# Optimization experiments

Hardware: AMD Instinct MI355X
Metric: run time of the kernel (lower is better)

The kernel has to match this reference:

```python
import jax, jax.numpy as jnp
import numpy as np

B, N, LQ, DK, DV, DD = 2, 16, 512, 64, 64, 128
TEMPERATURE = 8.0  # sqrt(DK)
NEG_INF = -1e9


def setup_inputs() -> dict:
    key = jax.random.key(0)
    ks = jax.random.split(key, 9)
    h2 = 2 * DD  # dc hidden width = d0 + d1
    return {
        "q": jax.random.normal(ks[0], (B, N, LQ, DK), jnp.float32),
        "k": jax.random.normal(ks[1], (B, N, LQ, DK), jnp.float32),
        "v": jax.random.normal(ks[2], (B, N, LQ, DV), jnp.float32),
        "d0": jax.random.normal(ks[3], (B, LQ, DD), jnp.float32),
        "d1": jax.random.normal(ks[4], (B, LQ, DD), jnp.float32),
        "W1": jax.random.normal(ks[5], (h2, h2), jnp.float32) / np.sqrt(h2),
        "b1": jnp.zeros((h2,), jnp.float32),
        "W2": jax.random.normal(ks[6], (h2, 2), jnp.float32) / np.sqrt(h2),
        "b2": jnp.zeros((2,), jnp.float32),
    }


def reference(q, k, v, d0, d1, W1, b1, W2, b2):
    b, n, lq, dk = q.shape
    dd = d0.shape[-1]
    # pairwise features: f[b,i,j] = concat(d0[b,i], d1[b,j])  -> [b,lq,lq,2dd]
    f = jnp.concatenate(
        [
            jnp.broadcast_to(d0[:, :, None, :], (b, lq, lq, dd)),
            jnp.broadcast_to(d1[:, None, :, :], (b, lq, lq, dd)),
        ],
        axis=-1,
    )
    h = jax.nn.relu(jnp.einsum("bijf,fg->bijg", f, W1) + b1)
    logits = jnp.einsum("bijg,gc->bijc", h, W2) + b2  # [b,lq,lq,2]
    # eval-mode gumbel_softmax(hard=True, tau=1, training=False): argmax of logits
    decisions = (jnp.argmax(logits, axis=-1) == 1)[:, None, :, :]  # [b,1,lq,lq]
    attn = jnp.einsum("bnid,bnjd->bnij", q / TEMPERATURE, k)
    attn = jnp.where(decisions, attn, NEG_INF)
    attn = jax.nn.softmax(attn, axis=-1)  # dropout is identity in eval mode
    output = jnp.einsum("bnij,bnjd->bnid", attn, v)
    return output, attn, decisions
```

## Files before the change

### kernel.cpp

```cpp
#include <hip/hip_runtime.h>

#define BB 2
#define NN 16
#define LQ 512
#define DKk 64
#define DVv 64
#define DDd 128
#define H2 256
#define NEG_INF -1e9f

__global__ __launch_bounds__(256) void mlp_stage1(
    const float* __restrict__ d0, const float* __restrict__ d1,
    const float* __restrict__ W1, const float* __restrict__ b1,
    double* __restrict__ U64, double* __restrict__ W64,
    float* __restrict__ U32, float* __restrict__ W32)
{
    __shared__ float drow[2][DDd];
    int gid = blockIdx.x;
    int half = gid >> 9;
    int r0 = (gid & 511) * 2;
    const float* din = half ? d1 : d0;
    int w1off = half ? DDd : 0;
    double* o64 = half ? W64 : U64;
    float* o32 = half ? W32 : U32;
    int t = threadIdx.x;
    drow[t >> 7][t & 127] = din[(size_t)(r0 + (t >> 7)) * DDd + (t & 127)];
    __syncthreads();
    int g = t;
    double acc[2] = {};
#pragma unroll 2
    for (int f = 0; f < DDd; f += 4) {
        double w0 = (double)W1[(w1off + f + 0) * H2 + g];
        double w1 = (double)W1[(w1off + f + 1) * H2 + g];
        double w2 = (double)W1[(w1off + f + 2) * H2 + g];
        double w3 = (double)W1[(w1off + f + 3) * H2 + g];
#pragma unroll
        for (int r = 0; r < 2; ++r) {
            float4 dr = *(const float4*)&drow[r][f];
            acc[r] = fma((double)dr.x, w0, acc[r]);
            acc[r] = fma((double)dr.y, w1, acc[r]);
            acc[r] = fma((double)dr.z, w2, acc[r]);
            acc[r] = fma((double)dr.w, w3, acc[r]);
        }
    }
    double bb = half ? 0.0 : (double)b1[g];
#pragma unroll
    for (int r = 0; r < 2; ++r) {
        double a = acc[r] + bb;
        o64[(size_t)(r0 + r) * H2 + g] = a;
        o32[(size_t)(r0 + r) * H2 + g] = (float)a;
    }
}

__global__ __launch_bounds__(256, 4) void dec_full(
    const float* __restrict__ U32, const float* __restrict__ W32,
    const double* __restrict__ U64, const double* __restrict__ W64,
    const float* __restrict__ W2, const float* __restrict__ b2,
    float* __restrict__ dec_out)
{
    __shared__ __align__(16) float Us[16][68];
    __shared__ __align__(16) float Ws[32][68];
    __shared__ __align__(16) float gvs[H2];
    __shared__ int lbuf[512];
    __shared__ int lcnt;
    int bid = blockIdx.x;
    int b  = bid >> 9;
    int i0 = ((bid >> 4) & 31) * 16;
    int j0 = (bid & 15) * 32;
    int t = threadIdx.x;
    gvs[t] = W2[t * 2 + 1] - W2[t * 2];
    if (t == 0) lcnt = 0;
    float bias = b2[1] - b2[0];
    int ti = t >> 4, tj = t & 15;
    float acc0 = 0.f, acc1 = 0.f;
    for (int gc = 0; gc < H2; gc += 64) {
        __syncthreads();
        {
            int ui = t >> 4, gq = t & 15;
            *(float4*)&Us[ui][gq * 4] =
                *(const float4*)(U32 + ((size_t)(b * LQ) + i0 + ui) * H2 + gc + gq * 4);
        }
        {
            int wj = t >> 3, gq = t & 7;
            const float* src = W32 + ((size_t)(b * LQ) + j0 + wj) * H2 + gc;
            *(float4*)&Ws[wj][gq * 4] = *(const float4*)(src + gq * 4);
            *(float4*)&Ws[wj][(gq + 8) * 4] = *(const float4*)(src + (gq + 8) * 4);
        }
        __syncthreads();
        float4 u_c  = *(const float4*)&Us[ti][0];
        float4 gv_c = *(const float4*)&gvs[gc];
        float4 wA_c = *(const float4*)&Ws[tj][0];
        float4 wB_c = *(const float4*)&Ws[tj + 16][0];
#pragma unroll 5
        for (int gg = 0; gg < 60; gg += 4) {
            float4 u_n  = *(const float4*)&Us[ti][gg + 4];
            float4 gv_n = *(const float4*)&gvs[gc + gg + 4];
            float4 wA_n = *(const float4*)&Ws[tj][gg + 4];
            float4 wB_n = *(const float4*)&Ws[tj + 16][gg + 4];
            acc0 = fmaf(fmaxf(u_c.x + wA_c.x, 0.f), gv_c.x, acc0);
            acc1 = fmaf(fmaxf(u_c.x + wB_c.x, 0.f), gv_c.x, acc1);
            acc0 = fmaf(fmaxf(u_c.y + wA_c.y, 0.f), gv_c.y, acc0);
            acc1 = fmaf(fmaxf(u_c.y + wB_c.y, 0.f), gv_c.y, acc1);
            acc0 = fmaf(fmaxf(u_c.z + wA_c.z, 0.f), gv_c.z, acc0);
            acc1 = fmaf(fmaxf(u_c.z + wB_c.z, 0.f), gv_c.z, acc1);
            acc0 = fmaf(fmaxf(u_c.w + wA_c.w, 0.f), gv_c.w, acc0);
            acc1 = fmaf(fmaxf(u_c.w + wB_c.w, 0.f), gv_c.w, acc1);
            u_c = u_n; gv_c = gv_n; wA_c = wA_n; wB_c = wB_n;
        }
        acc0 = fmaf(fmaxf(u_c.x + wA_c.x, 0.f), gv_c.x, acc0);
        acc1 = fmaf(fmaxf(u_c.x + wB_c.x, 0.f), gv_c.x, acc1);
        acc0 = fmaf(fmaxf(u_c.y + wA_c.y, 0.f), gv_c.y, acc0);
        acc1 = fmaf(fmaxf(u_c.y + wB_c.y, 0.f), gv_c.y, acc1);
        acc0 = fmaf(fmaxf(u_c.z + wA_c.z, 0.f), gv_c.z, acc0);
        acc1 = fmaf(fmaxf(u_c.z + wB_c.z, 0.f), gv_c.z, acc1);
        acc0 = fmaf(fmaxf(u_c.w + wA_c.w, 0.f), gv_c.w, acc0);
        acc1 = fmaf(fmaxf(u_c.w + wB_c.w, 0.f), gv_c.w, acc1);
    }
    int row = b * LQ + i0 + ti;
    float gA = acc0 + bias, gB = acc1 + bias;
    int jA = j0 + tj, jB = j0 + tj + 16;
    dec_out[(size_t)row * LQ + jA] = gA > 0.f ? 1.f : 0.f;
    dec_out[(size_t)row * LQ + jB] = gB > 0.f ? 1.f : 0.f;
    if (fabsf(gA) < 2e-2f) { int lx = atomicAdd(&lcnt, 1); lbuf[lx] = (row << 9) | jA; }
    if (fabsf(gB) < 2e-2f) { int lx = atomicAdd(&lcnt, 1); lbuf[lx] = (row << 9) | jB; }
    __syncthreads();
    int nloc = lcnt;
    int wv = t >> 6, ln = t & 63;
    for (int x = wv; x < nloc; x += 4) {
        int pij = lbuf[x];
        int j = pij & (LQ - 1);
        int prow = pij >> 9;
        int pb = prow >> 9;
        const double* u = U64 + (size_t)prow * H2;
        const double* w = W64 + ((size_t)(pb * LQ) + j) * H2;
        double acc = 0.0;
        for (int g = ln; g < H2; g += 64) {
            double tv = u[g] + w[g];
            tv = tv > 0.0 ? tv : 0.0;
            acc = fma(tv, (double)W2[g * 2 + 1] - (double)W2[g * 2 + 0], acc);
        }
#pragma unroll
        for (int off = 32; off; off >>= 1) acc += __shfl_xor(acc, off, 64);
        if (ln == 0) {
            acc += (double)b2[1] - (double)b2[0];
            dec_out[(size_t)prow * LQ + j] = acc > 0.0 ? 1.f : 0.f;
        }
    }
}

__global__ __launch_bounds__(256) void fused_attn(
    const float* __restrict__ q, const float* __restrict__ k,
    const float* __restrict__ v, const float* __restrict__ dec,
    float* __restrict__ attn, float* __restrict__ out)
{
    __shared__ __align__(16) float smem[10752];
    float* qT = smem;
    float* kT = smem + 2304;
    float* Ps = smem;
    float* Vs = smem + 2112;
    int bid = blockIdx.x;
    int bn = bid >> 4;
    int i0 = (bid & 15) * 32;
    int b = bn >> 4;
    int t = threadIdx.x;

    {
        int qi = t >> 3;
        const float* src = q + ((size_t)bn * LQ + i0 + qi) * DKk;
#pragma unroll
        for (int it = 0; it < 2; ++it) {
            int kkq = (t & 7) + it * 8;
            float4 t4 = *(const float4*)(src + kkq * 4);
            qT[(kkq * 4 + 0) * 36 + qi] = t4.x;
            qT[(kkq * 4 + 1) * 36 + qi] = t4.y;
            qT[(kkq * 4 + 2) * 36 + qi] = t4.z;
            qT[(kkq * 4 + 3) * 36 + qi] = t4.w;
        }
    }
    int tiq = t >> 5;
    int tjq = t & 31;
    float s[4][4][4];

#pragma unroll
    for (int c = 0; c < 4; ++c) {
        __syncthreads();
        {
            int kj = t >> 2;
#pragma unroll
            for (int it = 0; it < 8; ++it) {
                int jj = kj + (it & 1) * 64;
                int kkq = (t & 3) + (it >> 1) * 4;
                float4 t4 = *(const float4*)(k + ((size_t)bn * LQ + c * 128 + jj) * DKk + kkq * 4);
                kT[(kkq * 4 + 0) * 132 + jj] = t4.x;
                kT[(kkq * 4 + 1) * 132 + jj] = t4.y;
                kT[(kkq * 4 + 2) * 132 + jj] = t4.z;
                kT[(kkq * 4 + 3) * 132 + jj] = t4.w;
            }
        }
        __syncthreads();
        float acc[4][4] = {};
#pragma unroll 8
        for (int kk = 0; kk < 64; ++kk) {
            float4 a  = *(const float4*)&qT[kk * 36 + tiq * 4];
            float4 bb = *(const float4*)&kT[kk * 132 + tjq * 4];
            acc[0][0] = fmaf(a.x, bb.x, acc[0][0]); acc[0][1] = fmaf(a.x, bb.y, acc[0][1]);
            acc[0][2] = fmaf(a.x, bb.z, acc[0][2]); acc[0][3] = fmaf(a.x, bb.w, acc[0][3]);
            acc[1][0] = fmaf(a.y, bb.x, acc[1][0]); acc[1][1] = fmaf(a.y, bb.y, acc[1][1]);
            acc[1][2] = fmaf(a.y, bb.z, acc[1][2]); acc[1][3] = fmaf(a.y, bb.w, acc[1][3]);
            acc[2][0] = fmaf(a.z, bb.x, acc[2][0]); acc[2][1] = fmaf(a.z, bb.y, acc[2][1]);
            acc[2][2] = fmaf(a.z, bb.z, acc[2][2]); acc[2][3] = fmaf(a.z, bb.w, acc[2][3]);
            acc[3][0] = fmaf(a.w, bb.x, acc[3][0]); acc[3][1] = fmaf(a.w, bb.y, acc[3][1]);
            acc[3][2] = fmaf(a.w, bb.z, acc[3][2]); acc[3][3] = fmaf(a.w, bb.w, acc[3][3]);
        }
#pragma unroll
        for (int r = 0; r < 4; ++r) {
            float4 m4 = *(const float4*)&dec[((size_t)(b * LQ) + i0 + tiq * 4 + r) * LQ + c * 128 + tjq * 4];
            s[c][r][0] = m4.x != 0.f ? acc[r][0] * 0.125f : NEG_INF;
            s[c][r][1] = m4.y != 0.f ? acc[r][1] * 0.125f : NEG_INF;
            s[c][r][2] = m4.z != 0.f ? acc[r][2] * 0.125f : NEG_INF;
            s[c][r][3] = m4.w != 0.f ? acc[r][3] * 0.125f : NEG_INF;
        }
    }
#pragma unroll
    for (int r = 0; r < 4; ++r) {
        float m = NEG_INF;
#pragma unroll
        for (int c = 0; c < 4; ++c)
#pragma unroll
            for (int cc = 0; cc < 4; ++cc) m = fmaxf(m, s[c][r][cc]);
#pragma unroll
        for (int off = 1; off < 32; off <<= 1) m = fmaxf(m, __shfl_xor(m, off, 32));
        float sum = 0.f;
#pragma unroll
        for (int c = 0; c < 4; ++c)
#pragma unroll
            for (int cc = 0; cc < 4; ++cc) {
                float e = __expf(s[c][r][cc] - m);
                s[c][r][cc] = e; sum += e;
            }
#pragma unroll
        for (int off = 1; off < 32; off <<= 1) sum += __shfl_xor(sum, off, 32);
        float inv = 1.f / sum;
#pragma unroll
        for (int c = 0; c < 4; ++c)
#pragma unroll
            for (int cc = 0; cc < 4; ++cc) s[c][r][cc] *= inv;
    }
#pragma unroll
    for (int c = 0; c < 4; ++c)
#pragma unroll
        for (int r = 0; r < 4; ++r) {
            float4 wv = make_float4(s[c][r][0], s[c][r][1], s[c][r][2], s[c][r][3]);
            *(float4*)&attn[((size_t)bn * LQ + i0 + tiq * 4 + r) * LQ + c * 128 + tjq * 4] = wv;
        }
    int tio = t >> 4;
    int tdo = t & 15;
    float o[2][4] = {};
#pragma unroll
    for (int c8 = 0; c8 < 8; ++c8) {
        __syncthreads();
        if ((tjq >> 4) == (c8 & 1)) {
            int jl4 = tjq & 15;
            int c = c8 >> 1;
#pragma unroll
            for (int r = 0; r < 4; ++r)
#pragma unroll
                for (int cc = 0; cc < 4; ++cc)
                    Ps[(tiq * 4 + r) * 65 + jl4 * 4 + cc] = s[c][r][cc];
        }
        {
            int vj = t >> 2;
#pragma unroll
            for (int it = 0; it < 4; ++it) {
                int dq = (t & 3) + it * 4;
                *(float4*)&Vs[vj * 68 + dq * 4] =
                    *(const float4*)(v + ((size_t)bn * LQ + c8 * 64 + vj) * DVv + dq * 4);
            }
        }
        __syncthreads();
#pragma unroll 8
        for (int jj = 0; jj < 64; ++jj) {
            float p0 = Ps[(tio * 2 + 0) * 65 + jj];
            float p1 = Ps[(tio * 2 + 1) * 65 + jj];
            float4 v4 = *(const float4*)&Vs[jj * 68 + tdo * 4];
            o[0][0] = fmaf(p0, v4.x, o[0][0]); o[0][1] = fmaf(p0, v4.y, o[0][1]);
            o[0][2] = fmaf(p0, v4.z, o[0][2]); o[0][3] = fmaf(p0, v4.w, o[0][3]);
            o[1][0] = fmaf(p1, v4.x, o[1][0]); o[1][1] = fmaf(p1, v4.y, o[1][1]);
            o[1][2] = fmaf(p1, v4.z, o[1][2]); o[1][3] = fmaf(p1, v4.w, o[1][3]);
        }
    }
#pragma unroll
    for (int rr = 0; rr < 2; ++rr)
        *(float4*)&out[((size_t)bn * LQ + i0 + tio * 2 + rr) * DVv + tdo * 4] =
            make_float4(o[rr][0], o[rr][1], o[rr][2], o[rr][3]);
}

extern "C" void kernel_launch(void* const* d_in, const int* in_sizes, int n_in,
                              void* d_out, int out_size, void* d_ws, size_t ws_size,
                              hipStream_t stream)
{
    const float* q  = (const float*)d_in[0];
    const float* k  = (const float*)d_in[1];
    const float* v  = (const float*)d_in[2];
    const float* d0 = (const float*)d_in[3];
    const float* d1 = (const float*)d_in[4];
    const float* W1 = (const float*)d_in[5];
    const float* b1 = (const float*)d_in[6];
    const float* W2 = (const float*)d_in[7];
    const float* b2 = (const float*)d_in[8];

    float* out  = (float*)d_out;
    float* attn = out + (size_t)BB * NN * LQ * DVv;
    float* dec  = attn + (size_t)BB * NN * LQ * LQ;

    char* scratch = (char*)attn;
    double* U64 = (double*)(scratch);
    double* W64 = (double*)(scratch + (2u << 20));
    float*  U32 = (float*) (scratch + (4u << 20));
    float*  W32 = (float*) (scratch + (5u << 20));

    mlp_stage1<<<1024, 256, 0, stream>>>(d0, d1, W1, b1, U64, W64, U32, W32);
    dec_full<<<1024, 256, 0, stream>>>(U32, W32, U64, W64, W2, b2, dec);
    fused_attn<<<512, 256, 0, stream>>>(q, k, v, dec, attn, out);
}
```

Measured before the change: 156.0 us.

## Retile pairwise decision kernel to 32x32 tiles with 2x2 register blocking

The decision kernel now covers a 32x32 (i,j) tile per block instead of 16x32. The full 256-wide U and W slices are loaded once into transposed shared memory, and each thread computes a 2x2 block of outputs. This halves the grid, removes the chunked reload loop and its barriers, and increases reuse of each shared load, which targets LDS bandwidth per FMA. In exchange, shared memory use grows to about 80KB per block and the occupancy hint drops to 2, and the transposed stores may cause bank conflicts.

```diff
diff --git a/kernel.cpp b/kernel.cpp
--- a/kernel.cpp
+++ b/kernel.cpp
@@ -52,77 +52,65 @@
     }
 }
 
-__global__ __launch_bounds__(256, 4) void dec_full(
+__global__ __launch_bounds__(256, 2) void dec_full(
     const float* __restrict__ U32, const float* __restrict__ W32,
     const double* __restrict__ U64, const double* __restrict__ W64,
     const float* __restrict__ W2, const float* __restrict__ b2,
     float* __restrict__ dec_out)
 {
-    __shared__ __align__(16) float Us[16][68];
-    __shared__ __align__(16) float Ws[32][68];
-    __shared__ __align__(16) float gvs[H2];
-    __shared__ int lbuf[512];
+    __shared__ __align__(16) float Ut[H2][36];
+    __shared__ __align__(16) float Wt[H2][36];
+    __shared__ float gvs[H2];
+    __shared__ int lbuf[1024];
     __shared__ int lcnt;
     int bid = blockIdx.x;
-    int b  = bid >> 9;
-    int i0 = ((bid >> 4) & 31) * 16;
+    int b  = bid >> 8;
+    int i0 = ((bid >> 4) & 15) * 32;
     int j0 = (bid & 15) * 32;
     int t = threadIdx.x;
     gvs[t] = W2[t * 2 + 1] - W2[t * 2];
     if (t == 0) lcnt = 0;
     float bias = b2[1] - b2[0];
-    int ti = t >> 4, tj = t & 15;
-    float acc0 = 0.f, acc1 = 0.f;
-    for (int gc = 0; gc < H2; gc += 64) {
-        __syncthreads();
-        {
-            int ui = t >> 4, gq = t & 15;
-            *(float4*)&Us[ui][gq * 4] =
-                *(const float4*)(U32 + ((size_t)(b * LQ) + i0 + ui) * H2 + gc + gq * 4);
-        }
-        {
-            int wj = t >> 3, gq = t & 7;
-            const float* src = W32 + ((size_t)(b * LQ) + j0 + wj) * H2 + gc;
-            *(float4*)&Ws[wj][gq * 4] = *(const float4*)(src + gq * 4);
-            *(float4*)&Ws[wj][(gq + 8) * 4] = *(const float4*)(src + (gq + 8) * 4);
-        }
-        __syncthreads();
-        float4 u_c  = *(const float4*)&Us[ti][0];
-        float4 gv_c = *(const float4*)&gvs[gc];
-        float4 wA_c = *(const float4*)&Ws[tj][0];
-        float4 wB_c = *(const float4*)&Ws[tj + 16][0];
-#pragma unroll 5
-        for (int gg = 0; gg < 60; gg += 4) {
-            float4 u_n  = *(const float4*)&Us[ti][gg + 4];
-            float4 gv_n = *(const float4*)&gvs[gc + gg + 4];
-            float4 wA_n = *(const float4*)&Ws[tj][gg + 4];
-            float4 wB_n = *(const float4*)&Ws[tj + 16][gg + 4];
-            acc0 = fmaf(fmaxf(u_c.x + wA_c.x, 0.f), gv_c.x, acc0);
-            acc1 = fmaf(fmaxf(u_c.x + wB_c.x, 0.f), gv_c.x, acc1);
-            acc0 = fmaf(fmaxf(u_c.y + wA_c.y, 0.f), gv_c.y, acc0);
-            acc1 = fmaf(fmaxf(u_c.y + wB_c.y, 0.f), gv_c.y, acc1);
-            acc0 = fmaf(fmaxf(u_c.z + wA_c.z, 0.f), gv_c.z, acc0);
-            acc1 = fmaf(fmaxf(u_c.z + wB_c.z, 0.f), gv_c.z, acc1);
-            acc0 = fmaf(fmaxf(u_c.w + wA_c.w, 0.f), gv_c.w, acc0);
-            acc1 = fmaf(fmaxf(u_c.w + wB_c.w, 0.f), gv_c.w, acc1);
-            u_c = u_n; gv_c = gv_n; wA_c = wA_n; wB_c = wB_n;
-        }
-        acc0 = fmaf(fmaxf(u_c.x + wA_c.x, 0.f), gv_c.x, acc0);
-        acc1 = fmaf(fmaxf(u_c.x + wB_c.x, 0.f), gv_c.x, acc1);
-        acc0 = fmaf(fmaxf(u_c.y + wA_c.y, 0.f), gv_c.y, acc0);
-        acc1 = fmaf(fmaxf(u_c.y + wB_c.y, 0.f), gv_c.y, acc1);
-        acc0 = fmaf(fmaxf(u_c.z + wA_c.z, 0.f), gv_c.z, acc0);
-        acc1 = fmaf(fmaxf(u_c.z + wB_c.z, 0.f), gv_c.z, acc1);
-        acc0 = fmaf(fmaxf(u_c.w + wA_c.w, 0.f), gv_c.w, acc0);
-        acc1 = fmaf(fmaxf(u_c.w + wB_c.w, 0.f), gv_c.w, acc1);
-    }
-    int row = b * LQ + i0 + ti;
-    float gA = acc0 + bias, gB = acc1 + bias;
-    int jA = j0 + tj, jB = j0 + tj + 16;
-    dec_out[(size_t)row * LQ + jA] = gA > 0.f ? 1.f : 0.f;
-    dec_out[(size_t)row * LQ + jB] = gB > 0.f ? 1.f : 0.f;
-    if (fabsf(gA) < 2e-2f) { int lx = atomicAdd(&lcnt, 1); lbuf[lx] = (row << 9) | jA; }
-    if (fabsf(gB) < 2e-2f) { int lx = atomicAdd(&lcnt, 1); lbuf[lx] = (row << 9) | jB; }
+    {
+        int r = t >> 3, gq = t & 7;
+        const float* su = U32 + ((size_t)(b * LQ) + i0 + r) * H2;
+        const float* sw = W32 + ((size_t)(b * LQ) + j0 + r) * H2;
+#pragma unroll
+        for (int s = 0; s < 8; ++s) {
+            int g = gq * 4 + s * 32;
+            float4 u4 = *(const float4*)(su + g);
+            Ut[g + 0][r] = u4.x; Ut[g + 1][r] = u4.y;
+            Ut[g + 2][r] = u4.z; Ut[g + 3][r] = u4.w;
+            float4 w4 = *(const float4*)(sw + g);
+            Wt[g + 0][r] = w4.x; Wt[g + 1][r] = w4.y;
+            Wt[g + 2][r] = w4.z; Wt[g + 3][r] = w4.w;
+        }
+    }
+    __syncthreads();
+    int pi = t >> 4, pj = t & 15;
+    float a00 = 0.f, a01 = 0.f, a10 = 0.f, a11 = 0.f;
+#pragma unroll 8
+    for (int g = 0; g < H2; ++g) {
+        float2 u2 = *(const float2*)&Ut[g][pi * 2];
+        float2 w2 = *(const float2*)&Wt[g][pj * 2];
+        float gv = gvs[g];
+        a00 = fmaf(fmaxf(u2.x + w2.x, 0.f), gv, a00);
+        a01 = fmaf(fmaxf(u2.x + w2.y, 0.f), gv, a01);
+        a10 = fmaf(fmaxf(u2.y + w2.x, 0.f), gv, a10);
+        a11 = fmaf(fmaxf(u2.y + w2.y, 0.f), gv, a11);
+    }
+    int row0 = b * LQ + i0 + pi * 2;
+    float g00 = a00 + bias, g01 = a01 + bias;
+    float g10 = a10 + bias, g11 = a11 + bias;
+    int jb = j0 + pj * 2;
+    *(float2*)&dec_out[(size_t)row0 * LQ + jb] =
+        make_float2(g00 > 0.f ? 1.f : 0.f, g01 > 0.f ? 1.f : 0.f);
+    *(float2*)&dec_out[(size_t)(row0 + 1) * LQ + jb] =
+        make_float2(g10 > 0.f ? 1.f : 0.f, g11 > 0.f ? 1.f : 0.f);
+    if (fabsf(g00) < 2e-2f) { int lx = atomicAdd(&lcnt, 1); lbuf[lx] = (row0 << 9) | jb; }
+    if (fabsf(g01) < 2e-2f) { int lx = atomicAdd(&lcnt, 1); lbuf[lx] = (row0 << 9) | (jb + 1); }
+    if (fabsf(g10) < 2e-2f) { int lx = atomicAdd(&lcnt, 1); lbuf[lx] = ((row0 + 1) << 9) | jb; }
+    if (fabsf(g11) < 2e-2f) { int lx = atomicAdd(&lcnt, 1); lbuf[lx] = ((row0 + 1) << 9) | (jb + 1); }
     __syncthreads();
     int nloc = lcnt;
     int wv = t >> 6, ln = t & 63;
@@ -320,6 +308,6 @@
     float*  W32 = (float*) (scratch + (5u << 20));
 
     mlp_stage1<<<1024, 256, 0, stream>>>(d0, d1, W1, b1, U64, W64, U32, W32);
-    dec_full<<<1024, 256, 0, stream>>>(U32, W32, U64, W64, W2, b2, dec);
+    dec_full<<<512, 256, 0, stream>>>(U32, W32, U64, W64, W2, b2, dec);
     fused_attn<<<512, 256, 0, stream>>>(q, k, v, dec, attn, out);
 }
```

Measured after the change: 166.2 us. 6.5% more time.
